# Optimization experiments

Hardware: AMD Instinct MI355X
Metric: run time of the kernel (lower is better)

The kernel has to match this reference:

```python
import jax, jax.numpy as jnp
import numpy as np

N = 50000          # num nodes
DEG = 16           # fixed degree (uniform CSR)
E = N * DEG        # num edges
R = 8              # num relations
IN = 128
HID = 128
OUT = 40
BN_EPS = 1e-5


def setup_inputs() -> dict:
    key = jax.random.key(0)
    k = jax.random.split(key, 5)
    x = jax.random.normal(k[0], (N, IN), jnp.float32)
    # glorot-ish init for per-relation weights
    W1 = jax.random.normal(k[1], (R, IN, HID), jnp.float32) * (2.0 / (IN + HID)) ** 0.5
    W2 = jax.random.normal(k[2], (R, HID, OUT), jnp.float32) * (2.0 / (HID + OUT)) ** 0.5
    ptr = jnp.arange(N + 1, dtype=jnp.int32) * DEG            # CSR row offsets
    idx = jax.random.randint(k[3], (E,), 0, N, jnp.int32)     # neighbor (src) ids
    edge_types = jax.random.randint(k[4], (E,), 0, R, jnp.int32)
    return {
        "x": x, "W1": W1, "W2": W2,
        "bn_gamma": jnp.ones((HID,), jnp.float32),
        "bn_beta": jnp.zeros((HID,), jnp.float32),
        "bn_mean": jnp.zeros((HID,), jnp.float32),
        "bn_var": jnp.ones((HID,), jnp.float32),
        "ptr": ptr, "idx": idx, "edge_types": edge_types,
    }


def _rgcn_layer(h, W, ptr, idx, edge_types):
    # RGCNOP: out[i] = sum_{e in [ptr[i],ptr[i+1])} x[idx[e]] @ W[etype[e]]
    # Efficient form: transform every node by every relation once, then gather
    # the (src, etype) pair per edge and scatter-add into destinations.
    xr = jnp.einsum('nd,rdh->nrh', h, W)             # [N, R, H]
    msgs = xr[idx, edge_types]                       # [E, H] irregular gather
    deg = ptr[1:] - ptr[:-1]                         # [N]
    dst = jnp.repeat(jnp.arange(ptr.shape[0] - 1, dtype=jnp.int32), deg,
                     total_repeat_length=idx.shape[0])
    agg = jax.ops.segment_sum(msgs, dst, num_segments=ptr.shape[0] - 1)
    return agg / deg[:, None].astype(agg.dtype)      # degree normalization


def reference(x, W1, W2, bn_gamma, bn_beta, bn_mean, bn_var, ptr, idx, edge_types):
    h = _rgcn_layer(x, W1, ptr, idx, edge_types)
    # BatchNorm1d in eval mode (history_size=0, dropout inactive)
    h = (h - bn_mean) * jax.lax.rsqrt(bn_var + BN_EPS) * bn_gamma + bn_beta
    h = jax.nn.relu(h)
    h = _rgcn_layer(h, W2, ptr, idx, edge_types)
    return jax.nn.log_softmax(h, axis=-1)
```

## Files before the change

kernel.cpp:

```cpp
#include <hip/hip_runtime.h>
#include <math.h>

typedef __attribute__((ext_vector_type(8))) short bf16x8;
typedef __attribute__((ext_vector_type(4))) float f32x4;

constexpr int kN   = 50000;
constexpr int kR   = 8;
constexpr int kIn  = 128;
constexpr int kHid = 128;
constexpr int kOut = 40;
constexpr int kNT  = 16;
constexpr int kLds = 1032;
constexpr float kBnEps = 1e-5f;

__device__ inline float bf2f(ushort s) { return __uint_as_float(((uint)s) << 16); }

__device__ __forceinline__ uint cvtpk(float a, float b) {
    uint r;
    asm("v_cvt_pk_bf16_f32 %0, %1, %2" : "=v"(r) : "v"(a), "v"(b));
    return r;
}

__device__ __forceinline__ void pack_unit(const float* __restrict__ W,
                                          ushort* __restrict__ dst,
                                          int N, int frag, int lane)
{
    const int kt = frag & 31;
    const int nt = frag >> 5;
    const int n  = nt * 16 + (lane & 15);
    const int q  = lane >> 4;
    float f[8];
    #pragma unroll
    for (int j = 0; j < 8; ++j) {
        const int k = kt * 32 + q * 8 + j;
        f[j] = (n < N) ? W[(size_t)k * N + n] : 0.f;
    }
    const size_t o = ((size_t)frag * 64 + lane) * 8;
    *(uint4*)&dst[o] = make_uint4(cvtpk(f[0], f[1]), cvtpk(f[2], f[3]),
                                  cvtpk(f[4], f[5]), cvtpk(f[6], f[7]));
}

__global__ __launch_bounds__(256)
void prep(const float* __restrict__ x,  ushort* __restrict__ xb,
          const float* __restrict__ W1, ushort* __restrict__ W1hi,
          const float* __restrict__ W2, ushort* __restrict__ W2hi)
{
    const int b   = blockIdx.x;
    const int tid = threadIdx.x;
    if (b < 3125) {
        const size_t i = ((size_t)b * 256 + tid) * 8;
        const float4 v0 = *(const float4*)&x[i];
        const float4 v1 = *(const float4*)&x[i + 4];
        *(uint4*)&xb[i] = make_uint4(cvtpk(v0.x, v0.y), cvtpk(v0.z, v0.w),
                                     cvtpk(v1.x, v1.y), cvtpk(v1.z, v1.w));
    } else if (b < 3125 + 64) {
        pack_unit(W1, W1hi, kHid, (b - 3125) * 4 + (tid >> 6), tid & 63);
    } else {
        const int frag = (b - 3189) * 4 + (tid >> 6);
        if (frag < 96) pack_unit(W2, W2hi, kOut, frag, tid & 63);
    }
}

#define ACCUM_ET(ET, VX, VY)                                                   \
    if ((ET) < 4) {                                                            \
        if ((ET) < 2) {                                                        \
            if ((ET) == 0) { a0.x += (VX); a0.y += (VY); }                     \
            else           { a1.x += (VX); a1.y += (VY); }                     \
        } else {                                                               \
            if ((ET) == 2) { a2.x += (VX); a2.y += (VY); }                     \
            else           { a3.x += (VX); a3.y += (VY); }                     \
        }                                                                      \
    } else {                                                                   \
        if ((ET) < 6) {                                                        \
            if ((ET) == 4) { a4.x += (VX); a4.y += (VY); }                     \
            else           { a5.x += (VX); a5.y += (VY); }                     \
        } else {                                                               \
            if ((ET) == 6) { a6.x += (VX); a6.y += (VY); }                     \
            else           { a7.x += (VX); a7.y += (VY); }                     \
        }                                                                      \
    }

#define RD(V, J) __builtin_amdgcn_readlane((V), (J))

#define G(BV, VI, J)                                                           \
    const ushort2 BV = *(const ushort2*)&feat[(size_t)RD(VI, J) * 128 + d2];

#define ACCUM_EDGE(VE, J, BV)                                                  \
    { const int et = RD(VE, J);                                                \
      const float vx = bf2f(BV.x), vy = bf2f(BV.y);                            \
      ACCUM_ET(et, vx, vy) }

#define ZERO_ACC                                                               \
    float2 a0 = {0.f,0.f}, a1 = {0.f,0.f}, a2 = {0.f,0.f}, a3 = {0.f,0.f};     \
    float2 a4 = {0.f,0.f}, a5 = {0.f,0.f}, a6 = {0.f,0.f}, a7 = {0.f,0.f};

#define STORE8(NN)                                                             \
    { const int nloc = (NN);                                                   \
      *(uint*)&aggHi[nloc][0 * 128 + d2] = cvtpk(a0.x, a0.y);                  \
      *(uint*)&aggHi[nloc][1 * 128 + d2] = cvtpk(a1.x, a1.y);                  \
      *(uint*)&aggHi[nloc][2 * 128 + d2] = cvtpk(a2.x, a2.y);                  \
      *(uint*)&aggHi[nloc][3 * 128 + d2] = cvtpk(a3.x, a3.y);                  \
      *(uint*)&aggHi[nloc][4 * 128 + d2] = cvtpk(a4.x, a4.y);                  \
      *(uint*)&aggHi[nloc][5 * 128 + d2] = cvtpk(a5.x, a5.y);                  \
      *(uint*)&aggHi[nloc][6 * 128 + d2] = cvtpk(a6.x, a6.y);                  \
      *(uint*)&aggHi[nloc][7 * 128 + d2] = cvtpk(a7.x, a7.y); }

#define KEEP16(B0,B1,B2,B3,B4,B5,B6,B7,B8,B9,B10,B11,B12,B13,B14,B15)          \
    asm volatile("" :: "v"(B0),"v"(B1),"v"(B2),"v"(B3),                        \
                       "v"(B4),"v"(B5),"v"(B6),"v"(B7),                        \
                       "v"(B8),"v"(B9),"v"(B10),"v"(B11),                      \
                       "v"(B12),"v"(B13),"v"(B14),"v"(B15));

__device__ __forceinline__ void phaseA_bf16(const ushort* __restrict__ feat,
                                            const int* __restrict__ ptr,
                                            const int* __restrict__ idx,
                                            const int* __restrict__ etype,
                                            int base, ushort (*aggHi)[kLds])
{
    const int lane = threadIdx.x & 63;
    const int wid  = threadIdx.x >> 6;
    const int d2   = lane * 2;

    const int node0 = base + wid * 2;
    const int p0 = ptr[node0];
    const int p1 = ptr[node0 + 1];
    const int p2 = ptr[node0 + 2];

    if (((p1 - p0) == 16) & ((p2 - p1) == 16)) {
        const int vi0 = idx[p0 + (lane & 15)];
        const int ve0 = etype[p0 + (lane & 15)];
        const int vi1 = idx[p1 + (lane & 15)];
        const int ve1 = etype[p1 + (lane & 15)];

        G(b0,  vi0, 0)  G(b1,  vi0, 1)  G(b2,  vi0, 2)  G(b3,  vi0, 3)
        G(b4,  vi0, 4)  G(b5,  vi0, 5)  G(b6,  vi0, 6)  G(b7,  vi0, 7)
        G(b8,  vi0, 8)  G(b9,  vi0, 9)  G(b10, vi0, 10) G(b11, vi0, 11)
        G(b12, vi0, 12) G(b13, vi0, 13) G(b14, vi0, 14) G(b15, vi0, 15)
        G(c0,  vi1, 0)  G(c1,  vi1, 1)  G(c2,  vi1, 2)  G(c3,  vi1, 3)
        G(c4,  vi1, 4)  G(c5,  vi1, 5)  G(c6,  vi1, 6)  G(c7,  vi1, 7)
        G(c8,  vi1, 8)  G(c9,  vi1, 9)  G(c10, vi1, 10) G(c11, vi1, 11)
        G(c12, vi1, 12) G(c13, vi1, 13) G(c14, vi1, 14) G(c15, vi1, 15)

        KEEP16(b0,b1,b2,b3,b4,b5,b6,b7,b8,b9,b10,b11,b12,b13,b14,b15)
        KEEP16(c0,c1,c2,c3,c4,c5,c6,c7,c8,c9,c10,c11,c12,c13,c14,c15)

        {
            ZERO_ACC
            ACCUM_EDGE(ve0, 0,  b0)  ACCUM_EDGE(ve0, 1,  b1)
            ACCUM_EDGE(ve0, 2,  b2)  ACCUM_EDGE(ve0, 3,  b3)
            ACCUM_EDGE(ve0, 4,  b4)  ACCUM_EDGE(ve0, 5,  b5)
            ACCUM_EDGE(ve0, 6,  b6)  ACCUM_EDGE(ve0, 7,  b7)
            ACCUM_EDGE(ve0, 8,  b8)  ACCUM_EDGE(ve0, 9,  b9)
            ACCUM_EDGE(ve0, 10, b10) ACCUM_EDGE(ve0, 11, b11)
            ACCUM_EDGE(ve0, 12, b12) ACCUM_EDGE(ve0, 13, b13)
            ACCUM_EDGE(ve0, 14, b14) ACCUM_EDGE(ve0, 15, b15)
            STORE8(wid * 2)
        }
        {
            ZERO_ACC
            ACCUM_EDGE(ve1, 0,  c0)  ACCUM_EDGE(ve1, 1,  c1)
            ACCUM_EDGE(ve1, 2,  c2)  ACCUM_EDGE(ve1, 3,  c3)
            ACCUM_EDGE(ve1, 4,  c4)  ACCUM_EDGE(ve1, 5,  c5)
            ACCUM_EDGE(ve1, 6,  c6)  ACCUM_EDGE(ve1, 7,  c7)
            ACCUM_EDGE(ve1, 8,  c8)  ACCUM_EDGE(ve1, 9,  c9)
            ACCUM_EDGE(ve1, 10, c10) ACCUM_EDGE(ve1, 11, c11)
            ACCUM_EDGE(ve1, 12, c12) ACCUM_EDGE(ve1, 13, c13)
            ACCUM_EDGE(ve1, 14, c14) ACCUM_EDGE(ve1, 15, c15)
            STORE8(wid * 2 + 1)
        }
    } else {
        #pragma unroll
        for (int t = 0; t < 2; ++t) {
            const int node = node0 + t;
            const int pa   = ptr[node];
            const int deg  = ptr[node + 1] - pa;
            ZERO_ACC
            for (int e = pa; e < pa + deg; ++e) {
                const int src = __builtin_amdgcn_readfirstlane(idx[e]);
                const int et  = __builtin_amdgcn_readfirstlane(etype[e]);
                const ushort2 u = *(const ushort2*)&feat[(size_t)src * 128 + d2];
                const float vx = bf2f(u.x), vy = bf2f(u.y);
                ACCUM_ET(et, vx, vy)
            }
            STORE8(wid * 2 + t)
        }
    }
}

__global__ __launch_bounds__(512, 4)
void rgcn_layer1(const ushort* __restrict__ xb,
                 const ushort* __restrict__ W1hi,
                 const float* __restrict__ gamma, const float* __restrict__ beta,
                 const float* __restrict__ mean,  const float* __restrict__ var,
                 const int* __restrict__ ptr, const int* __restrict__ idx,
                 const int* __restrict__ etype,
                 ushort* __restrict__ h1b)
{
    __shared__ ushort aggHi[kNT][kLds];
    const int tid  = threadIdx.x;
    const int base = blockIdx.x * kNT;

    phaseA_bf16(xb, ptr, idx, etype, base, aggHi);
    __syncthreads();

    const int lane = tid & 63;
    const int wid  = tid >> 6;
    const int m    = lane & 15;
    const int q    = lane >> 4;

    const bf16x8* Bh = (const bf16x8*)W1hi + (size_t)wid * 32 * 64 + lane;
    f32x4 acc = {0.f, 0.f, 0.f, 0.f};

    #pragma unroll 4
    for (int kt = 0; kt < 32; ++kt) {
        const bf16x8 ah = *(const bf16x8*)&aggHi[m][kt * 32 + q * 8];
        const bf16x8 bh = Bh[(size_t)kt * 64];
        acc = __builtin_amdgcn_mfma_f32_16x16x32_bf16(ah, bh, acc, 0, 0, 0);
    }

    const int c = wid * 16 + m;
    const float g  = gamma[c] * rsqrtf(var[c] + kBnEps);
    const float mu = mean[c];
    const float bt = beta[c];
    float v[4];
    #pragma unroll
    for (int i = 0; i < 4; ++i) {
        const int node = base + q * 4 + i;
        const float invdeg = 1.0f / (float)(ptr[node + 1] - ptr[node]);
        v[i] = fmaxf((acc[i] * invdeg - mu) * g + bt, 0.f);
    }
    const uint p01 = cvtpk(v[0], v[1]);
    const uint p23 = cvtpk(v[2], v[3]);
    const int n0 = base + q * 4;
    h1b[(size_t)(n0 + 0) * kHid + c] = (ushort)(p01 & 0xFFFFu);
    h1b[(size_t)(n0 + 1) * kHid + c] = (ushort)(p01 >> 16);
    h1b[(size_t)(n0 + 2) * kHid + c] = (ushort)(p23 & 0xFFFFu);
    h1b[(size_t)(n0 + 3) * kHid + c] = (ushort)(p23 >> 16);
}

__global__ __launch_bounds__(512, 4)
void rgcn_layer2(const ushort* __restrict__ h1b,
                 const ushort* __restrict__ W2hi,
                 const int* __restrict__ ptr, const int* __restrict__ idx,
                 const int* __restrict__ etype,
                 float* __restrict__ out)
{
    __shared__ ushort aggHi[kNT][kLds];
    __shared__ float logits[kNT][48];
    const int tid  = threadIdx.x;
    const int base = blockIdx.x * kNT;

    phaseA_bf16(h1b, ptr, idx, etype, base, aggHi);
    __syncthreads();

    const int lane = tid & 63;
    const int wid  = tid >> 6;
    const int m    = lane & 15;
    const int q    = lane >> 4;

    if (wid < 3) {
        const bf16x8* Bh = (const bf16x8*)W2hi + (size_t)wid * 32 * 64 + lane;
        f32x4 acc = {0.f, 0.f, 0.f, 0.f};
        #pragma unroll 4
        for (int kt = 0; kt < 32; ++kt) {
            const bf16x8 ah = *(const bf16x8*)&aggHi[m][kt * 32 + q * 8];
            const bf16x8 bh = Bh[(size_t)kt * 64];
            acc = __builtin_amdgcn_mfma_f32_16x16x32_bf16(ah, bh, acc, 0, 0, 0);
        }
        const int n = wid * 16 + m;
        if (n < kOut) {
            #pragma unroll
            for (int i = 0; i < 4; ++i) {
                const int node = base + q * 4 + i;
                const float invdeg = 1.0f / (float)(ptr[node + 1] - ptr[node]);
                logits[q * 4 + i][n] = acc[i] * invdeg;
            }
        }
    }
    __syncthreads();

    #pragma unroll
    for (int i = 0; i < 2; ++i) {
        const int nrow = wid * 2 + i;
        const int node = base + nrow;
        const float v = (lane < kOut) ? logits[nrow][lane] : -INFINITY;
        float mx = v;
        #pragma unroll
        for (int off = 32; off > 0; off >>= 1)
            mx = fmaxf(mx, __shfl_xor(mx, off, 64));
        float s = (lane < kOut) ? __expf(v - mx) : 0.f;
        #pragma unroll
        for (int off = 32; off > 0; off >>= 1)
            s += __shfl_xor(s, off, 64);
        if (lane < kOut)
            out[(size_t)node * kOut + lane] = v - mx - __logf(s);
    }
}

extern "C" void kernel_launch(void* const* d_in, const int* in_sizes, int n_in,
                              void* d_out, int out_size, void* d_ws, size_t ws_size,
                              hipStream_t stream)
{
    const float* x     = (const float*)d_in[0];
    const float* W1    = (const float*)d_in[1];
    const float* W2    = (const float*)d_in[2];
    const float* gamma = (const float*)d_in[3];
    const float* beta  = (const float*)d_in[4];
    const float* mean  = (const float*)d_in[5];
    const float* var   = (const float*)d_in[6];
    const int*   ptr   = (const int*)d_in[7];
    const int*   idx   = (const int*)d_in[8];
    const int*   et    = (const int*)d_in[9];
    float*       out   = (float*)d_out;

    char* ws = (char*)d_ws;
    ushort* h1b  = (ushort*)ws;
    ushort* xb   = (ushort*)(ws + 12800000);
    ushort* W1hi = (ushort*)(ws + 25600000);
    ushort* W2hi = (ushort*)(ws + 25600000 + 262144);

    prep<<<dim3(3125 + 64 + 24), dim3(256), 0, stream>>>(x, xb, W1, W1hi, W2, W2hi);

    dim3 grid(kN / kNT), block(512);
    rgcn_layer1<<<grid, block, 0, stream>>>(xb, W1hi, gamma, beta, mean, var,
                                            ptr, idx, et, h1b);
    rgcn_layer2<<<grid, block, 0, stream>>>(h1b, W2hi, ptr, idx, et, out);
}
```

Before: 216.7 us.

## Double node tile to 32 per block with 1024 threads and restructure gather

```diff
diff --git a/kernel.cpp b/kernel.cpp
--- a/kernel.cpp
+++ b/kernel.cpp
@@ -9,7 +9,7 @@
 constexpr int kIn  = 128;
 constexpr int kHid = 128;
 constexpr int kOut = 40;
-constexpr int kNT  = 16;
+constexpr int kNT  = 32;
 constexpr int kLds = 1032;
 constexpr float kBnEps = 1e-5f;
 
@@ -82,8 +82,8 @@
 
 #define RD(V, J) __builtin_amdgcn_readlane((V), (J))
 
-#define G(BV, VI, J)                                                           \
-    const ushort2 BV = *(const ushort2*)&feat[(size_t)RD(VI, J) * 128 + d2];
+#define GATHER(BV, SRC) \
+    const ushort2 BV = *(const ushort2*)&feat[(size_t)(SRC) * 128 + d2];
 
 #define ACCUM_EDGE(VE, J, BV)                                                  \
     { const int et = RD(VE, J);                                                \
@@ -105,11 +105,31 @@
       *(uint*)&aggHi[nloc][6 * 128 + d2] = cvtpk(a6.x, a6.y);                  \
       *(uint*)&aggHi[nloc][7 * 128 + d2] = cvtpk(a7.x, a7.y); }
 
-#define KEEP16(B0,B1,B2,B3,B4,B5,B6,B7,B8,B9,B10,B11,B12,B13,B14,B15)          \
-    asm volatile("" :: "v"(B0),"v"(B1),"v"(B2),"v"(B3),                        \
-                       "v"(B4),"v"(B5),"v"(B6),"v"(B7),                        \
-                       "v"(B8),"v"(B9),"v"(B10),"v"(B11),                      \
-                       "v"(B12),"v"(B13),"v"(B14),"v"(B15));
+#define NODE_BODY(VI, VE, NLOC)                                                \
+    {                                                                          \
+        const int s0  = RD(VI, 0);  const int s1  = RD(VI, 1);                 \
+        const int s2  = RD(VI, 2);  const int s3  = RD(VI, 3);                 \
+        const int s4  = RD(VI, 4);  const int s5  = RD(VI, 5);                 \
+        const int s6  = RD(VI, 6);  const int s7  = RD(VI, 7);                 \
+        const int s8  = RD(VI, 8);  const int s9  = RD(VI, 9);                 \
+        const int s10 = RD(VI, 10); const int s11 = RD(VI, 11);                \
+        const int s12 = RD(VI, 12); const int s13 = RD(VI, 13);                \
+        const int s14 = RD(VI, 14); const int s15 = RD(VI, 15);                \
+        GATHER(b0,  s0)  GATHER(b1,  s1)  GATHER(b2,  s2)  GATHER(b3,  s3)     \
+        GATHER(b4,  s4)  GATHER(b5,  s5)  GATHER(b6,  s6)  GATHER(b7,  s7)     \
+        GATHER(b8,  s8)  GATHER(b9,  s9)  GATHER(b10, s10) GATHER(b11, s11)    \
+        GATHER(b12, s12) GATHER(b13, s13) GATHER(b14, s14) GATHER(b15, s15)    \
+        ZERO_ACC                                                               \
+        ACCUM_EDGE(VE, 0,  b0)  ACCUM_EDGE(VE, 1,  b1)                         \
+        ACCUM_EDGE(VE, 2,  b2)  ACCUM_EDGE(VE, 3,  b3)                         \
+        ACCUM_EDGE(VE, 4,  b4)  ACCUM_EDGE(VE, 5,  b5)                         \
+        ACCUM_EDGE(VE, 6,  b6)  ACCUM_EDGE(VE, 7,  b7)                         \
+        ACCUM_EDGE(VE, 8,  b8)  ACCUM_EDGE(VE, 9,  b9)                         \
+        ACCUM_EDGE(VE, 10, b10) ACCUM_EDGE(VE, 11, b11)                        \
+        ACCUM_EDGE(VE, 12, b12) ACCUM_EDGE(VE, 13, b13)                        \
+        ACCUM_EDGE(VE, 14, b14) ACCUM_EDGE(VE, 15, b15)                        \
+        STORE8(NLOC)                                                           \
+    }
 
 __device__ __forceinline__ void phaseA_bf16(const ushort* __restrict__ feat,
                                             const int* __restrict__ ptr,
@@ -122,6 +142,7 @@
     const int d2   = lane * 2;
 
     const int node0 = base + wid * 2;
+    if (node0 >= kN) return;
     const int p0 = ptr[node0];
     const int p1 = ptr[node0 + 1];
     const int p2 = ptr[node0 + 2];
@@ -131,43 +152,8 @@
         const int ve0 = etype[p0 + (lane & 15)];
         const int vi1 = idx[p1 + (lane & 15)];
         const int ve1 = etype[p1 + (lane & 15)];
-
-        G(b0,  vi0, 0)  G(b1,  vi0, 1)  G(b2,  vi0, 2)  G(b3,  vi0, 3)
-        G(b4,  vi0, 4)  G(b5,  vi0, 5)  G(b6,  vi0, 6)  G(b7,  vi0, 7)
-        G(b8,  vi0, 8)  G(b9,  vi0, 9)  G(b10, vi0, 10) G(b11, vi0, 11)
-        G(b12, vi0, 12) G(b13, vi0, 13) G(b14, vi0, 14) G(b15, vi0, 15)
-        G(c0,  vi1, 0)  G(c1,  vi1, 1)  G(c2,  vi1, 2)  G(c3,  vi1, 3)
-        G(c4,  vi1, 4)  G(c5,  vi1, 5)  G(c6,  vi1, 6)  G(c7,  vi1, 7)
-        G(c8,  vi1, 8)  G(c9,  vi1, 9)  G(c10, vi1, 10) G(c11, vi1, 11)
-        G(c12, vi1, 12) G(c13, vi1, 13) G(c14, vi1, 14) G(c15, vi1, 15)
-
-        KEEP16(b0,b1,b2,b3,b4,b5,b6,b7,b8,b9,b10,b11,b12,b13,b14,b15)
-        KEEP16(c0,c1,c2,c3,c4,c5,c6,c7,c8,c9,c10,c11,c12,c13,c14,c15)
-
-        {
-            ZERO_ACC
-            ACCUM_EDGE(ve0, 0,  b0)  ACCUM_EDGE(ve0, 1,  b1)
-            ACCUM_EDGE(ve0, 2,  b2)  ACCUM_EDGE(ve0, 3,  b3)
-            ACCUM_EDGE(ve0, 4,  b4)  ACCUM_EDGE(ve0, 5,  b5)
-            ACCUM_EDGE(ve0, 6,  b6)  ACCUM_EDGE(ve0, 7,  b7)
-            ACCUM_EDGE(ve0, 8,  b8)  ACCUM_EDGE(ve0, 9,  b9)
-            ACCUM_EDGE(ve0, 10, b10) ACCUM_EDGE(ve0, 11, b11)
-            ACCUM_EDGE(ve0, 12, b12) ACCUM_EDGE(ve0, 13, b13)
-            ACCUM_EDGE(ve0, 14, b14) ACCUM_EDGE(ve0, 15, b15)
-            STORE8(wid * 2)
-        }
-        {
-            ZERO_ACC
-            ACCUM_EDGE(ve1, 0,  c0)  ACCUM_EDGE(ve1, 1,  c1)
-            ACCUM_EDGE(ve1, 2,  c2)  ACCUM_EDGE(ve1, 3,  c3)
-            ACCUM_EDGE(ve1, 4,  c4)  ACCUM_EDGE(ve1, 5,  c5)
-            ACCUM_EDGE(ve1, 6,  c6)  ACCUM_EDGE(ve1, 7,  c7)
-            ACCUM_EDGE(ve1, 8,  c8)  ACCUM_EDGE(ve1, 9,  c9)
-            ACCUM_EDGE(ve1, 10, c10) ACCUM_EDGE(ve1, 11, c11)
-            ACCUM_EDGE(ve1, 12, c12) ACCUM_EDGE(ve1, 13, c13)
-            ACCUM_EDGE(ve1, 14, c14) ACCUM_EDGE(ve1, 15, c15)
-            STORE8(wid * 2 + 1)
-        }
+        NODE_BODY(vi0, ve0, wid * 2)
+        NODE_BODY(vi1, ve1, wid * 2 + 1)
     } else {
         #pragma unroll
         for (int t = 0; t < 2; ++t) {
@@ -187,7 +173,7 @@
     }
 }
 
-__global__ __launch_bounds__(512, 4)
+__global__ __launch_bounds__(1024, 4)
 void rgcn_layer1(const ushort* __restrict__ xb,
                  const ushort* __restrict__ W1hi,
                  const float* __restrict__ gamma, const float* __restrict__ beta,
@@ -207,38 +193,41 @@
     const int wid  = tid >> 6;
     const int m    = lane & 15;
     const int q    = lane >> 4;
-
-    const bf16x8* Bh = (const bf16x8*)W1hi + (size_t)wid * 32 * 64 + lane;
+    const int ni   = wid & 7;
+    const int mi   = wid >> 3;
+
+    const bf16x8* Bh = (const bf16x8*)W1hi + (size_t)ni * 32 * 64 + lane;
     f32x4 acc = {0.f, 0.f, 0.f, 0.f};
 
     #pragma unroll 4
     for (int kt = 0; kt < 32; ++kt) {
-        const bf16x8 ah = *(const bf16x8*)&aggHi[m][kt * 32 + q * 8];
+        const bf16x8 ah = *(const bf16x8*)&aggHi[mi * 16 + m][kt * 32 + q * 8];
         const bf16x8 bh = Bh[(size_t)kt * 64];
         acc = __builtin_amdgcn_mfma_f32_16x16x32_bf16(ah, bh, acc, 0, 0, 0);
     }
 
-    const int c = wid * 16 + m;
+    const int c = ni * 16 + m;
     const float g  = gamma[c] * rsqrtf(var[c] + kBnEps);
     const float mu = mean[c];
     const float bt = beta[c];
+    const int n0 = base + mi * 16 + q * 4;
     float v[4];
     #pragma unroll
     for (int i = 0; i < 4; ++i) {
-        const int node = base + q * 4 + i;
-        const float invdeg = 1.0f / (float)(ptr[node + 1] - ptr[node]);
+        const int node = n0 + i;
+        float invdeg = 1.0f;
+        if (node < kN) invdeg = 1.0f / (float)(ptr[node + 1] - ptr[node]);
         v[i] = fmaxf((acc[i] * invdeg - mu) * g + bt, 0.f);
     }
     const uint p01 = cvtpk(v[0], v[1]);
     const uint p23 = cvtpk(v[2], v[3]);
-    const int n0 = base + q * 4;
-    h1b[(size_t)(n0 + 0) * kHid + c] = (ushort)(p01 & 0xFFFFu);
-    h1b[(size_t)(n0 + 1) * kHid + c] = (ushort)(p01 >> 16);
-    h1b[(size_t)(n0 + 2) * kHid + c] = (ushort)(p23 & 0xFFFFu);
-    h1b[(size_t)(n0 + 3) * kHid + c] = (ushort)(p23 >> 16);
-}
-
-__global__ __launch_bounds__(512, 4)
+    if (n0 + 0 < kN) h1b[(size_t)(n0 + 0) * kHid + c] = (ushort)(p01 & 0xFFFFu);
+    if (n0 + 1 < kN) h1b[(size_t)(n0 + 1) * kHid + c] = (ushort)(p01 >> 16);
+    if (n0 + 2 < kN) h1b[(size_t)(n0 + 2) * kHid + c] = (ushort)(p23 & 0xFFFFu);
+    if (n0 + 3 < kN) h1b[(size_t)(n0 + 3) * kHid + c] = (ushort)(p23 >> 16);
+}
+
+__global__ __launch_bounds__(1024, 4)
 void rgcn_layer2(const ushort* __restrict__ h1b,
                  const ushort* __restrict__ W2hi,
                  const int* __restrict__ ptr, const int* __restrict__ idx,
@@ -258,22 +247,26 @@
     const int m    = lane & 15;
     const int q    = lane >> 4;
 
-    if (wid < 3) {
-        const bf16x8* Bh = (const bf16x8*)W2hi + (size_t)wid * 32 * 64 + lane;
+    if (wid < 6) {
+        const int ni = wid >> 1;
+        const int mi = wid & 1;
+        const bf16x8* Bh = (const bf16x8*)W2hi + (size_t)ni * 32 * 64 + lane;
         f32x4 acc = {0.f, 0.f, 0.f, 0.f};
         #pragma unroll 4
         for (int kt = 0; kt < 32; ++kt) {
-            const bf16x8 ah = *(const bf16x8*)&aggHi[m][kt * 32 + q * 8];
+            const bf16x8 ah = *(const bf16x8*)&aggHi[mi * 16 + m][kt * 32 + q * 8];
             const bf16x8 bh = Bh[(size_t)kt * 64];
             acc = __builtin_amdgcn_mfma_f32_16x16x32_bf16(ah, bh, acc, 0, 0, 0);
         }
-        const int n = wid * 16 + m;
+        const int n = ni * 16 + m;
         if (n < kOut) {
             #pragma unroll
             for (int i = 0; i < 4; ++i) {
-                const int node = base + q * 4 + i;
-                const float invdeg = 1.0f / (float)(ptr[node + 1] - ptr[node]);
-                logits[q * 4 + i][n] = acc[i] * invdeg;
+                const int node = base + mi * 16 + q * 4 + i;
+                if (node < kN) {
+                    const float invdeg = 1.0f / (float)(ptr[node + 1] - ptr[node]);
+                    logits[mi * 16 + q * 4 + i][n] = acc[i] * invdeg;
+                }
             }
         }
     }
@@ -283,17 +276,19 @@
     for (int i = 0; i < 2; ++i) {
         const int nrow = wid * 2 + i;
         const int node = base + nrow;
-        const float v = (lane < kOut) ? logits[nrow][lane] : -INFINITY;
-        float mx = v;
-        #pragma unroll
-        for (int off = 32; off > 0; off >>= 1)
-            mx = fmaxf(mx, __shfl_xor(mx, off, 64));
-        float s = (lane < kOut) ? __expf(v - mx) : 0.f;
-        #pragma unroll
-        for (int off = 32; off > 0; off >>= 1)
-            s += __shfl_xor(s, off, 64);
-        if (lane < kOut)
-            out[(size_t)node * kOut + lane] = v - mx - __logf(s);
+        if (node < kN) {
+            const float v = (lane < kOut) ? logits[nrow][lane] : -INFINITY;
+            float mx = v;
+            #pragma unroll
+            for (int off = 32; off > 0; off >>= 1)
+                mx = fmaxf(mx, __shfl_xor(mx, off, 64));
+            float s = (lane < kOut) ? __expf(v - mx) : 0.f;
+            #pragma unroll
+            for (int off = 32; off > 0; off >>= 1)
+                s += __shfl_xor(s, off, 64);
+            if (lane < kOut)
+                out[(size_t)node * kOut + lane] = v - mx - __logf(s);
+        }
     }
 }
 
@@ -321,8 +316,8 @@
 
     prep<<<dim3(3125 + 64 + 24), dim3(256), 0, stream>>>(x, xb, W1, W1hi, W2, W2hi);
 
-    dim3 grid(kN / kNT), block(512);
-    rgcn_layer1<<<grid, block, 0, stream>>>(xb, W1hi, gamma, beta, mean, var,
-                                            ptr, idx, et, h1b);
-    rgcn_layer2<<<grid, block, 0, stream>>>(h1b, W2hi, ptr, idx, et, out);
-}
+    const int grid = (kN + kNT - 1) / kNT;
+    rgcn_layer1<<<dim3(grid), dim3(1024), 0, stream>>>(xb, W1hi, gamma, beta, mean, var,
+                                                       ptr, idx, et, h1b);
+    rgcn_layer2<<<dim3(grid), dim3(1024), 0, stream>>>(h1b, W2hi, ptr, idx, et, out);
+}
```

Measured after the change: 199.7 us. -7.8%, faster.

## Aggregate per-relation edge messages with one-hot MFMA instead of branchy VALU accumulation

Applied to the files above, without the earlier changes.

```diff
diff --git a/kernel.cpp b/kernel.cpp
--- a/kernel.cpp
+++ b/kernel.cpp
@@ -5,7 +5,6 @@
 typedef __attribute__((ext_vector_type(4))) float f32x4;
 
 constexpr int kN   = 50000;
-constexpr int kR   = 8;
 constexpr int kIn  = 128;
 constexpr int kHid = 128;
 constexpr int kOut = 40;
@@ -14,6 +13,12 @@
 constexpr float kBnEps = 1e-5f;
 
 __device__ inline float bf2f(ushort s) { return __uint_as_float(((uint)s) << 16); }
+
+__device__ __forceinline__ ushort f2bf(float x) {
+    uint u = __float_as_uint(x);
+    u += 0x7FFFu + ((u >> 16) & 1u);
+    return (ushort)(u >> 16);
+}
 
 __device__ __forceinline__ uint cvtpk(float a, float b) {
     uint r;
@@ -61,130 +66,128 @@
     }
 }
 
-#define ACCUM_ET(ET, VX, VY)                                                   \
-    if ((ET) < 4) {                                                            \
-        if ((ET) < 2) {                                                        \
-            if ((ET) == 0) { a0.x += (VX); a0.y += (VY); }                     \
-            else           { a1.x += (VX); a1.y += (VY); }                     \
-        } else {                                                               \
-            if ((ET) == 2) { a2.x += (VX); a2.y += (VY); }                     \
-            else           { a3.x += (VX); a3.y += (VY); }                     \
-        }                                                                      \
-    } else {                                                                   \
-        if ((ET) < 6) {                                                        \
-            if ((ET) == 4) { a4.x += (VX); a4.y += (VY); }                     \
-            else           { a5.x += (VX); a5.y += (VY); }                     \
-        } else {                                                               \
-            if ((ET) == 6) { a6.x += (VX); a6.y += (VY); }                     \
-            else           { a7.x += (VX); a7.y += (VY); }                     \
-        }                                                                      \
-    }
-
-#define RD(V, J) __builtin_amdgcn_readlane((V), (J))
-
-#define G(BV, VI, J)                                                           \
-    const ushort2 BV = *(const ushort2*)&feat[(size_t)RD(VI, J) * 128 + d2];
-
-#define ACCUM_EDGE(VE, J, BV)                                                  \
-    { const int et = RD(VE, J);                                                \
-      const float vx = bf2f(BV.x), vy = bf2f(BV.y);                            \
-      ACCUM_ET(et, vx, vy) }
-
-#define ZERO_ACC                                                               \
-    float2 a0 = {0.f,0.f}, a1 = {0.f,0.f}, a2 = {0.f,0.f}, a3 = {0.f,0.f};     \
-    float2 a4 = {0.f,0.f}, a5 = {0.f,0.f}, a6 = {0.f,0.f}, a7 = {0.f,0.f};
-
-#define STORE8(NN)                                                             \
-    { const int nloc = (NN);                                                   \
-      *(uint*)&aggHi[nloc][0 * 128 + d2] = cvtpk(a0.x, a0.y);                  \
-      *(uint*)&aggHi[nloc][1 * 128 + d2] = cvtpk(a1.x, a1.y);                  \
-      *(uint*)&aggHi[nloc][2 * 128 + d2] = cvtpk(a2.x, a2.y);                  \
-      *(uint*)&aggHi[nloc][3 * 128 + d2] = cvtpk(a3.x, a3.y);                  \
-      *(uint*)&aggHi[nloc][4 * 128 + d2] = cvtpk(a4.x, a4.y);                  \
-      *(uint*)&aggHi[nloc][5 * 128 + d2] = cvtpk(a5.x, a5.y);                  \
-      *(uint*)&aggHi[nloc][6 * 128 + d2] = cvtpk(a6.x, a6.y);                  \
-      *(uint*)&aggHi[nloc][7 * 128 + d2] = cvtpk(a7.x, a7.y); }
-
-#define KEEP16(B0,B1,B2,B3,B4,B5,B6,B7,B8,B9,B10,B11,B12,B13,B14,B15)          \
-    asm volatile("" :: "v"(B0),"v"(B1),"v"(B2),"v"(B3),                        \
-                       "v"(B4),"v"(B5),"v"(B6),"v"(B7),                        \
-                       "v"(B8),"v"(B9),"v"(B10),"v"(B11),                      \
-                       "v"(B12),"v"(B13),"v"(B14),"v"(B15));
-
-__device__ __forceinline__ void phaseA_bf16(const ushort* __restrict__ feat,
+
+__device__ __forceinline__ void stage_fast(const char* fb, int vi, char* msW,
+                                           int hOff, int lane)
+{
+    const int b = (lane & 7) * 16;
+    #pragma unroll
+    for (int u = 0; u < 4; ++u) {
+        const int e   = u * 8 + (lane >> 3);
+        const int src = __shfl(vi, e, 64);
+        const uint4 v = *(const uint4*)(fb + (((size_t)(uint)src) << 8) + hOff + b);
+        *(uint4*)(msW + e * 128 + (b ^ (u << 5))) = v;
+    }
+}
+
+__device__ __forceinline__ void stage_slow(const char* fb,
+                                           const int* __restrict__ idx,
+                                           int p0, int p1, int deg0, int deg1,
+                                           char* msW, int hOff, int lane)
+{
+    const int l31 = lane & 31;
+    if (lane < 32) {
+        for (int e = 0; e < 32; ++e) {
+            const bool eok = (e < 16) ? (e < deg0) : ((e - 16) < deg1);
+            uint val = 0;
+            if (eok) {
+                const int g = (e < 16) ? (p0 + e) : (p1 + (e - 16));
+                const int s = idx[g];
+                val = *(const uint*)(fb + (((size_t)(uint)s) << 8) + hOff + l31 * 4);
+            }
+            *(uint*)(msW + e * 128 + ((l31 * 4) ^ (((e >> 3) & 3) << 5))) = val;
+        }
+    }
+}
+
+__device__ __forceinline__ bf16x8 readB(const char* msW, int q, int m, int ntL)
+{
+    const char* ap = msW + q * 1024 + 2 * m + (((ntL ^ q) & 3) << 5);
+    bf16x8 b;
+    #pragma unroll
+    for (int j = 0; j < 8; ++j) b[j] = *(const short*)(ap + j * 128);
+    return b;
+}
+
+__device__ __forceinline__ void mfma_store(bf16x8 aS, bf16x8 bb, int fbase,
+                                           int ntL, int w, int q, int m,
+                                           ushort (*aggHi)[kLds])
+{
+    f32x4 z = {0.f, 0.f, 0.f, 0.f};
+    const f32x4 d = __builtin_amdgcn_mfma_f32_16x16x32_bf16(aS, bb, z, 0, 0, 0);
+    ushort* dst = &aggHi[2 * w + (q >> 1)][0];
+    const int fcol = fbase + ntL * 16 + m;
+    const int rb   = (q & 1) * 4;
+    dst[(rb + 0) * 128 + fcol] = f2bf(d[0]);
+    dst[(rb + 1) * 128 + fcol] = f2bf(d[1]);
+    dst[(rb + 2) * 128 + fcol] = f2bf(d[2]);
+    dst[(rb + 3) * 128 + fcol] = f2bf(d[3]);
+}
+
+__device__ __forceinline__ void phaseA_mfma(const ushort* __restrict__ feat,
                                             const int* __restrict__ ptr,
                                             const int* __restrict__ idx,
                                             const int* __restrict__ etype,
-                                            int base, ushort (*aggHi)[kLds])
+                                            int base, ushort (*aggHi)[kLds],
+                                            char* msgs)
 {
     const int lane = threadIdx.x & 63;
-    const int wid  = threadIdx.x >> 6;
-    const int d2   = lane * 2;
-
-    const int node0 = base + wid * 2;
+    const int w    = threadIdx.x >> 6;
+    const int m    = lane & 15;
+    const int q    = lane >> 4;
+    const char* fb = (const char*)feat;
+
+    const int node0 = base + 2 * w;
     const int p0 = ptr[node0];
     const int p1 = ptr[node0 + 1];
     const int p2 = ptr[node0 + 2];
-
-    if (((p1 - p0) == 16) & ((p2 - p1) == 16)) {
-        const int vi0 = idx[p0 + (lane & 15)];
-        const int ve0 = etype[p0 + (lane & 15)];
-        const int vi1 = idx[p1 + (lane & 15)];
-        const int ve1 = etype[p1 + (lane & 15)];
-
-        G(b0,  vi0, 0)  G(b1,  vi0, 1)  G(b2,  vi0, 2)  G(b3,  vi0, 3)
-        G(b4,  vi0, 4)  G(b5,  vi0, 5)  G(b6,  vi0, 6)  G(b7,  vi0, 7)
-        G(b8,  vi0, 8)  G(b9,  vi0, 9)  G(b10, vi0, 10) G(b11, vi0, 11)
-        G(b12, vi0, 12) G(b13, vi0, 13) G(b14, vi0, 14) G(b15, vi0, 15)
-        G(c0,  vi1, 0)  G(c1,  vi1, 1)  G(c2,  vi1, 2)  G(c3,  vi1, 3)
-        G(c4,  vi1, 4)  G(c5,  vi1, 5)  G(c6,  vi1, 6)  G(c7,  vi1, 7)
-        G(c8,  vi1, 8)  G(c9,  vi1, 9)  G(c10, vi1, 10) G(c11, vi1, 11)
-        G(c12, vi1, 12) G(c13, vi1, 13) G(c14, vi1, 14) G(c15, vi1, 15)
-
-        KEEP16(b0,b1,b2,b3,b4,b5,b6,b7,b8,b9,b10,b11,b12,b13,b14,b15)
-        KEEP16(c0,c1,c2,c3,c4,c5,c6,c7,c8,c9,c10,c11,c12,c13,c14,c15)
-
-        {
-            ZERO_ACC
-            ACCUM_EDGE(ve0, 0,  b0)  ACCUM_EDGE(ve0, 1,  b1)
-            ACCUM_EDGE(ve0, 2,  b2)  ACCUM_EDGE(ve0, 3,  b3)
-            ACCUM_EDGE(ve0, 4,  b4)  ACCUM_EDGE(ve0, 5,  b5)
-            ACCUM_EDGE(ve0, 6,  b6)  ACCUM_EDGE(ve0, 7,  b7)
-            ACCUM_EDGE(ve0, 8,  b8)  ACCUM_EDGE(ve0, 9,  b9)
-            ACCUM_EDGE(ve0, 10, b10) ACCUM_EDGE(ve0, 11, b11)
-            ACCUM_EDGE(ve0, 12, b12) ACCUM_EDGE(ve0, 13, b13)
-            ACCUM_EDGE(ve0, 14, b14) ACCUM_EDGE(ve0, 15, b15)
-            STORE8(wid * 2)
-        }
-        {
-            ZERO_ACC
-            ACCUM_EDGE(ve1, 0,  c0)  ACCUM_EDGE(ve1, 1,  c1)
-            ACCUM_EDGE(ve1, 2,  c2)  ACCUM_EDGE(ve1, 3,  c3)
-            ACCUM_EDGE(ve1, 4,  c4)  ACCUM_EDGE(ve1, 5,  c5)
-            ACCUM_EDGE(ve1, 6,  c6)  ACCUM_EDGE(ve1, 7,  c7)
-            ACCUM_EDGE(ve1, 8,  c8)  ACCUM_EDGE(ve1, 9,  c9)
-            ACCUM_EDGE(ve1, 10, c10) ACCUM_EDGE(ve1, 11, c11)
-            ACCUM_EDGE(ve1, 12, c12) ACCUM_EDGE(ve1, 13, c13)
-            ACCUM_EDGE(ve1, 14, c14) ACCUM_EDGE(ve1, 15, c15)
-            STORE8(wid * 2 + 1)
-        }
+    const int deg0 = p1 - p0, deg1 = p2 - p1;
+    const bool fast = (deg0 == 16) && (deg1 == 16);
+
+    const int vi = idx  [p0 + (lane & 31)];
+    const int ve = etype[p0 + (lane & 31)];
+
+    char* msW = msgs + w * 4096;
+
+    int code;
+    if (fast) {
+        code = (((lane & 31) >> 4) << 3) | ve;
     } else {
-        #pragma unroll
-        for (int t = 0; t < 2; ++t) {
-            const int node = node0 + t;
-            const int pa   = ptr[node];
-            const int deg  = ptr[node + 1] - pa;
-            ZERO_ACC
-            for (int e = pa; e < pa + deg; ++e) {
-                const int src = __builtin_amdgcn_readfirstlane(idx[e]);
-                const int et  = __builtin_amdgcn_readfirstlane(etype[e]);
-                const ushort2 u = *(const ushort2*)&feat[(size_t)src * 128 + d2];
-                const float vx = bf2f(u.x), vy = bf2f(u.y);
-                ACCUM_ET(et, vx, vy)
-            }
-            STORE8(wid * 2 + t)
-        }
-    }
+        const int l31 = lane & 31;
+        const bool eok = (l31 < 16) ? (l31 < deg0) : ((l31 - 16) < deg1);
+        code = eok ? (((l31 >> 4) << 3) | ve) : 0xFF;
+    }
+
+    bf16x8 aS;
+    #pragma unroll
+    for (int j = 0; j < 8; ++j) {
+        const int cj = __shfl(code, q * 8 + j, 64);
+        aS[j] = (cj == m) ? (short)0x3F80 : (short)0;
+    }
+
+    if (fast) stage_fast(fb, vi, msW, 0, lane);
+    else      stage_slow(fb, idx, p0, p1, deg0, deg1, msW, 0, lane);
+    const bf16x8 b0 = readB(msW, q, m, 0);
+    const bf16x8 b1 = readB(msW, q, m, 1);
+    const bf16x8 b2 = readB(msW, q, m, 2);
+    const bf16x8 b3 = readB(msW, q, m, 3);
+
+    if (fast) stage_fast(fb, vi, msW, 128, lane);
+    else      stage_slow(fb, idx, p0, p1, deg0, deg1, msW, 128, lane);
+
+    mfma_store(aS, b0, 0, 0, w, q, m, aggHi);
+    mfma_store(aS, b1, 0, 1, w, q, m, aggHi);
+    mfma_store(aS, b2, 0, 2, w, q, m, aggHi);
+    mfma_store(aS, b3, 0, 3, w, q, m, aggHi);
+
+    const bf16x8 c0 = readB(msW, q, m, 0);
+    const bf16x8 c1 = readB(msW, q, m, 1);
+    const bf16x8 c2 = readB(msW, q, m, 2);
+    const bf16x8 c3 = readB(msW, q, m, 3);
+    mfma_store(aS, c0, 64, 0, w, q, m, aggHi);
+    mfma_store(aS, c1, 64, 1, w, q, m, aggHi);
+    mfma_store(aS, c2, 64, 2, w, q, m, aggHi);
+    mfma_store(aS, c3, 64, 3, w, q, m, aggHi);
 }
 
 __global__ __launch_bounds__(512, 4)
@@ -197,10 +200,11 @@
                  ushort* __restrict__ h1b)
 {
     __shared__ ushort aggHi[kNT][kLds];
+    __shared__ __align__(16) char msgs[8 * 4096];
     const int tid  = threadIdx.x;
     const int base = blockIdx.x * kNT;
 
-    phaseA_bf16(xb, ptr, idx, etype, base, aggHi);
+    phaseA_mfma(xb, ptr, idx, etype, base, aggHi, msgs);
     __syncthreads();
 
     const int lane = tid & 63;
@@ -246,11 +250,12 @@
                  float* __restrict__ out)
 {
     __shared__ ushort aggHi[kNT][kLds];
+    __shared__ __align__(16) char msgs[8 * 4096];
     __shared__ float logits[kNT][48];
     const int tid  = threadIdx.x;
     const int base = blockIdx.x * kNT;
 
-    phaseA_bf16(h1b, ptr, idx, etype, base, aggHi);
+    phaseA_mfma(h1b, ptr, idx, etype, base, aggHi, msgs);
     __syncthreads();
 
     const int lane = tid & 63;
```

Measured after the change: 196.6 us. -9.3%, faster.
